# Kernel tuning notes

Measured on AMD Instinct MI355X. Metric: run time of the kernel, lower is better.

## Reference

```python
import jax, jax.numpy as jnp
import numpy as np
from jax import lax

EPS = 1e-5
S_CENTROIDS = 2048
K_NEIGH = 32


def _fps(xyz, S):
    """Farthest point sampling. xyz: (B,N,3) -> idx (B,S) int32."""
    B, N, _ = xyz.shape

    def body(carry, _):
        dist, farthest = carry  # (B,N), (B,)
        centroid = jnp.take_along_axis(xyz, farthest[:, None, None], axis=1)  # (B,1,3)
        d = jnp.sum((xyz - centroid) ** 2, axis=-1)  # (B,N)
        dist = jnp.minimum(dist, d)
        nxt = jnp.argmax(dist, axis=-1).astype(jnp.int32)
        return (dist, nxt), farthest

    init = (jnp.full((B, N), 1e10, xyz.dtype), jnp.zeros((B,), jnp.int32))
    _, idx = lax.scan(body, init, None, length=S)
    return idx.T  # (B,S)


def _knn(q, p, K):
    """q: (B,S,3) queries, p: (B,N,3) points -> idx (B,S,K) of K nearest."""
    d = (jnp.sum(q * q, -1)[:, :, None] + jnp.sum(p * p, -1)[:, None, :]
         - 2.0 * jnp.einsum('bsd,bnd->bsn', q, p))  # (B,S,N) sq dists
    _, idx = lax.top_k(-d, K)
    return idx


def _mlp_layer(x, w, g, b, m, v):
    # x: (B,S,K,Cin); 1x1 conv == channel matmul, then eval-mode BN, then ReLU
    x = jnp.einsum('bskc,oc->bsko', x, w)
    x = (x - m) * (g * lax.rsqrt(v + EPS)) + b
    return jax.nn.relu(x)


def setup_inputs() -> dict:
    key = jax.random.key(0)
    ks = jax.random.split(key, 8)
    B, N, D = 4, 8192, 64
    inp = {
        'xyz': jax.random.normal(ks[0], (B, N, 3), jnp.float32),
        'points': jax.random.normal(ks[1], (B, D, N), jnp.float32),
        'w0': jax.random.normal(ks[2], (64, 67), jnp.float32) * (1.0 / np.sqrt(67)),
        'g0': jnp.ones((64,), jnp.float32), 'b0': jnp.zeros((64,), jnp.float32),
        'm0': jnp.zeros((64,), jnp.float32), 'v0': jnp.ones((64,), jnp.float32),
        'w1': jax.random.normal(ks[3], (64, 64), jnp.float32) * (1.0 / np.sqrt(64)),
        'g1': jnp.ones((64,), jnp.float32), 'b1': jnp.zeros((64,), jnp.float32),
        'm1': jnp.zeros((64,), jnp.float32), 'v1': jnp.ones((64,), jnp.float32),
        'w2': jax.random.normal(ks[4], (128, 64), jnp.float32) * (1.0 / np.sqrt(64)),
        'g2': jnp.ones((128,), jnp.float32), 'b2': jnp.zeros((128,), jnp.float32),
        'm2': jnp.zeros((128,), jnp.float32), 'v2': jnp.ones((128,), jnp.float32),
    }
    return inp


def reference(xyz, points, w0, g0, b0, m0, v0, w1, g1, b1, m1, v1,
              w2, g2, b2, m2, v2):
    B, N, _ = xyz.shape
    S, K = S_CENTROIDS, K_NEIGH

    # FPS centroids (S < N path of the module)
    fps_idx = _fps(xyz, S)                                        # (B,S)
    new_xyz = jnp.take_along_axis(xyz, fps_idx[..., None], axis=1)  # (B,S,3)

    # KNN grouping
    idx = _knn(new_xyz, xyz, K)                                   # (B,S,K)
    grouped_xyz = jnp.take_along_axis(xyz[:, None], idx[..., None], axis=2)  # (B,S,K,3)
    grouped_xyz = grouped_xyz - new_xyz[:, :, None, :]

    # gather neighbor features: points (B,D,N) -> (B,N,D) -> (B,S,K,D)
    pts = jnp.transpose(points, (0, 2, 1))
    neigh = jnp.take_along_axis(pts[:, None], idx[..., None], axis=2)
    grouped = jnp.concatenate([grouped_xyz, neigh], axis=-1)      # (B,S,K,3+D)

    x = _mlp_layer(grouped, w0, g0, b0, m0, v0)
    x = _mlp_layer(x, w1, g1, b1, m1, v1)
    x = _mlp_layer(x, w2, g2, b2, m2, v2)                         # (B,S,K,128)

    new_points = jnp.transpose(jnp.max(x, axis=2), (0, 2, 1))     # (B,128,S)
    return new_xyz, new_points
```

## Files before the change

### kernel.cpp

```cpp
#include <hip/hip_runtime.h>
#include <cfloat>
#include <climits>

#define NPTS   8192
#define SCENT  2048
#define KNEIGH 32
#define BATCH  4
#define DFEAT  64
#define FPS_T  512
#define NV     8
#define NW     8
#define CAP    64
#define NCONS  252
#define CPB    63

typedef float v2f __attribute__((ext_vector_type(2)));

#define DPPTOP2(um, us, ctrl, rmask)                                                  \
    { unsigned _tm = (unsigned)__builtin_amdgcn_update_dpp(0, (int)(um), (ctrl),      \
                                                           (rmask), 0xf, false);     \
      unsigned _ts = (unsigned)__builtin_amdgcn_update_dpp(0, (int)(us), (ctrl),      \
                                                           (rmask), 0xf, false);     \
      unsigned _lo = ((um) < _tm) ? (um) : _tm;                                       \
      (us) = ((us) > _ts) ? (us) : _ts;                                               \
      (us) = ((us) > _lo) ? (us) : _lo;                                               \
      (um) = ((um) > _tm) ? (um) : _tm; }

#define FLUSH_PUB(Eidx, VX, VY, VZ, HASPREV, PX, PY, PZ)                              \
    if (((Eidx) & 63) == 63) {                                                        \
        const int base0 = (Eidx) - 63;                                                \
        if (t < 64 * 3) {                                                             \
            const int ci = base0 + t / 3;                                             \
            const int cc = t - (t / 3) * 3;                                           \
            float v;                                                                  \
            if (ci == (Eidx))                                                         \
                v = (cc == 0) ? (VX) : ((cc == 1) ? (VY) : (VZ));                     \
            else if ((HASPREV) && ci == (Eidx) - 1)                                   \
                v = (cc == 0) ? (PX) : ((cc == 1) ? (PY) : (PZ));                     \
            else                                                                      \
                v = (cc == 0) ? S.hx[ci] : ((cc == 1) ? S.hy[ci] : S.hz[ci]);         \
            __hip_atomic_store(&new_xyz[((size_t)b * SCENT + base0) * 3 + t], v,      \
                               __ATOMIC_RELAXED, __HIP_MEMORY_SCOPE_AGENT);           \
        }                                                                             \
        __syncthreads();                 \
        if (t == 0)                                                                   \
            __hip_atomic_store(&progress[b], (Eidx) + 1,                              \
                               __ATOMIC_RELEASE, __HIP_MEMORY_SCOPE_AGENT);           \
    }

struct FpsSh {
    float sx[NPTS], sy[NPTS], sz[NPTS];
    float hx[SCENT], hy[SCENT], hz[SCENT];
    alignas(16) unsigned slotQ[2][NW][4];
    int scand[CAP];
    int scnt;
    alignas(8) double sdd[2][NW];
    double sfv[NW];
    int sfo[NW];
};
struct ConsSh {
    float  spx[2048], spy[2048], spz[2048];
    double sp2[2048];
    float  tile[32 * 33];
    float  regA[64 * 68];
    float  regB[64 * 64];
    float  regC[128 * 64];
    float  prm[512];
};
union ShU { FpsSh f; ConsSh c; };

__global__ __launch_bounds__(FPS_T, 1) void fused_kernel(
        const float* __restrict__ xyz, float* __restrict__ new_xyz,
        const float* __restrict__ pts, float* __restrict__ ptsT,
        int* __restrict__ progress, int* __restrict__ tcount,
        float* __restrict__ out_points,
        const float* __restrict__ w0, const float* __restrict__ g0,
        const float* __restrict__ b0, const float* __restrict__ m0,
        const float* __restrict__ v0, const float* __restrict__ w1,
        const float* __restrict__ g1, const float* __restrict__ b1,
        const float* __restrict__ m1, const float* __restrict__ v1,
        const float* __restrict__ w2, const float* __restrict__ g2,
        const float* __restrict__ b2, const float* __restrict__ m2,
        const float* __restrict__ v2) {
    __shared__ ShU sh;
    const int t = threadIdx.x;
    const int lane = t & 63, w = t >> 6;

    if (blockIdx.x < BATCH) {
        FpsSh& S = sh.f;
        const int b = blockIdx.x;
        const float* X = xyz + (size_t)b * NPTS * 3;

        for (int p = t; p < NPTS; p += FPS_T) {
            S.sx[p] = X[3 * p + 0]; S.sy[p] = X[3 * p + 1]; S.sz[p] = X[3 * p + 2];
        }

        v2f px2[NV], py2[NV], pz2[NV], dist2[NV];
#pragma unroll
        for (int j = 0; j < NV; ++j) {
            int pA = t + FPS_T * j, pB = t + FPS_T * (j + NV);
            px2[j] = (v2f){X[3 * pA + 0], X[3 * pB + 0]};
            py2[j] = (v2f){X[3 * pA + 1], X[3 * pB + 1]};
            pz2[j] = (v2f){X[3 * pA + 2], X[3 * pB + 2]};
            dist2[j] = (v2f){1e10f, 1e10f};
        }
        float c0x = X[0], c0y = X[1], c0z = X[2];
        float c1x = 0.f, c1y = 0.f, c1z = 0.f;
        int dual = 0, buf = 0;
        int E = 1;
        if (t == 0) { S.hx[0] = c0x; S.hy[0] = c0y; S.hz[0] = c0z; }
        __syncthreads();

#pragma unroll 1
        while (true) {
            float m2s = -1.f, s2s = -1.f;
            {
                const v2f cxx = {c0x, c0x}, cyy = {c0y, c0y}, czz = {c0z, c0z};
                if (dual) {
                    const v2f exx = {c1x, c1x}, eyy = {c1y, c1y}, ezz = {c1z, c1z};
#pragma unroll
                    for (int j = 0; j < NV; ++j) {
                        v2f dx = px2[j] - cxx, dy = py2[j] - cyy, dz = pz2[j] - czz;
                        v2f d0 = __builtin_elementwise_fma(dx, dx,
                                 __builtin_elementwise_fma(dy, dy, dz * dz));
                        v2f ex = px2[j] - exx, ey = py2[j] - eyy, ez = pz2[j] - ezz;
                        v2f d1 = __builtin_elementwise_fma(ex, ex,
                                 __builtin_elementwise_fma(ey, ey, ez * ez));
                        v2f d  = __builtin_elementwise_min(d0, d1);
                        v2f nd = __builtin_elementwise_min(dist2[j], d);
                        dist2[j] = nd;
                        float hi = fmaxf(nd.x, nd.y), lo = fminf(nd.x, nd.y);
                        s2s = fmaxf(fmaxf(s2s, lo), fminf(m2s, hi));
                        m2s = fmaxf(m2s, hi);
                    }
                } else {
#pragma unroll
                    for (int j = 0; j < NV; ++j) {
                        v2f dx = px2[j] - cxx, dy = py2[j] - cyy, dz = pz2[j] - czz;
                        v2f d  = __builtin_elementwise_fma(dx, dx,
                                 __builtin_elementwise_fma(dy, dy, dz * dz));
                        v2f nd = __builtin_elementwise_min(dist2[j], d);
                        dist2[j] = nd;
                        float hi = fmaxf(nd.x, nd.y), lo = fminf(nd.x, nd.y);
                        s2s = fmaxf(fmaxf(s2s, lo), fminf(m2s, hi));
                        m2s = fmaxf(m2s, hi);
                    }
                }
            }
            const float m = m2s, sec = s2s;

            int mi = 0;
#pragma unroll
            for (int j = 0; j < NV; ++j) {
                mi = (dist2[j].x == m) ? (t + FPS_T * j)        : mi;
                mi = (dist2[j].y == m) ? (t + FPS_T * (j + NV)) : mi;
            }

            const unsigned myU = __float_as_uint(m);
            unsigned um = myU, us = __float_as_uint(sec);
            DPPTOP2(um, us, 0x111, 0xf);
            DPPTOP2(um, us, 0x112, 0xf);
            DPPTOP2(um, us, 0x114, 0xf);
            DPPTOP2(um, us, 0x118, 0xf);
            DPPTOP2(um, us, 0x142, 0xa);
            DPPTOP2(um, us, 0x143, 0xc);
            const unsigned wu  = (unsigned)__builtin_amdgcn_readlane((int)um, 63);
            const unsigned wsu = (unsigned)__builtin_amdgcn_readlane((int)us, 63);

            unsigned long long wb = __ballot(myU == wu);
            const int wl   = __ffsll(wb) - 1;
            const int widx = __builtin_amdgcn_readlane(mi, wl);
            const float thwf = __fmul_rn(__uint_as_float(wu), 0.999998f);
            const unsigned tw = (__uint_as_float(wsu) >= thwf) ? 1u : 0u;
            if (lane == 0) {
                *(uint4*)&S.slotQ[buf][w][0] =
                    make_uint4(wu, (unsigned)widx | (tw << 14), wsu, 0u);
            }
            __syncthreads();

            unsigned mv[NW], mt4[NW], sv2[NW];
            {
                const uint4* qp = (const uint4*)&S.slotQ[buf][0][0];
                uint4 u0 = qp[0], u1 = qp[1], u2 = qp[2], u3 = qp[3];
                uint4 u4 = qp[4], u5 = qp[5], u6 = qp[6], u7 = qp[7];
                mv[0]=u0.x; mt4[0]=u0.y; sv2[0]=u0.z;
                mv[1]=u1.x; mt4[1]=u1.y; sv2[1]=u1.z;
                mv[2]=u2.x; mt4[2]=u2.y; sv2[2]=u2.z;
                mv[3]=u3.x; mt4[3]=u3.y; sv2[3]=u3.z;
                mv[4]=u4.x; mt4[4]=u4.y; sv2[4]=u4.z;
                mv[5]=u5.x; mt4[5]=u5.y; sv2[5]=u5.z;
                mv[6]=u6.x; mt4[6]=u6.y; sv2[6]=u6.z;
                mv[7]=u7.x; mt4[7]=u7.y; sv2[7]=u7.z;
            }
            unsigned gu = mv[0];
#pragma unroll
            for (int k = 1; k < NW; ++k) gu = (mv[k] > gu) ? mv[k] : gu;
            const float gvf  = __uint_as_float(gu);
            const float gthf = __fmul_rn(gvf, 0.999998f);
            const unsigned ugth = __float_as_uint(gthf);
            int nw = 0; unsigned meta = 0; int kw = 0;
#pragma unroll
            for (int k = NW - 1; k >= 0; --k) {
                nw  += (mv[k] >= ugth) ? 1 : 0;
                meta = (mv[k] == gu) ? mt4[k] : meta;
                kw   = (mv[k] == gu) ? k : kw;
            }
            const int wtie = (meta >> 14) & 1;
            int i1 = (int)(meta & 0x3fffu);
            const int fb = (nw >= 2) || wtie;

            if (fb) {
                if (t == 0) S.scnt = 0;
                __syncthreads();
#pragma unroll
                for (int j = 0; j < NV; ++j) {
                    if (dist2[j].x >= gthf) {
                        int slot = atomicAdd(&S.scnt, 1);
                        if (slot < CAP) S.scand[slot] = t + FPS_T * j;
                    }
                    if (dist2[j].y >= gthf) {
                        int slot = atomicAdd(&S.scnt, 1);
                        if (slot < CAP) S.scand[slot] = t + FPS_T * (j + NV);
                    }
                }
                __syncthreads();
                const int mm = S.scnt;
                if (mm <= CAP) {
                    double bd = -1.0; int bi = INT_MAX;
#pragma unroll 1
                    for (int k = 0; k < mm; ++k) {
                        const int pos = S.scand[k];
                        const double pxd = (double)S.sx[pos], pyd = (double)S.sy[pos],
                                     pzd = (double)S.sz[pos];
                        double dd = 1e10;
                        for (int i = t; i < E; i += FPS_T) {
                            double ddx = __dsub_rn(pxd, (double)S.hx[i]);
                            double ddy = __dsub_rn(pyd, (double)S.hy[i]);
                            double ddz = __dsub_rn(pzd, (double)S.hz[i]);
                            double d = __dadd_rn(__dadd_rn(__dmul_rn(ddx, ddx), __dmul_rn(ddy, ddy)),
                                                 __dmul_rn(ddz, ddz));
                            dd = fmin(dd, d);
                        }
#pragma unroll
                        for (int off = 32; off >= 1; off >>= 1)
                            dd = fmin(dd, __shfl_down(dd, off));
                        if (lane == 0) S.sdd[k & 1][w] = dd;
                        __syncthreads();
                        double ddm = S.sdd[k & 1][0];
#pragma unroll
                        for (int w2i = 1; w2i < NW; ++w2i) ddm = fmin(ddm, S.sdd[k & 1][w2i]);
                        if (ddm > bd || (ddm == bd && pos < bi)) { bd = ddm; bi = pos; }
                    }
                    i1 = bi;
                } else {
                    double bv = -1.0; int bi = INT_MAX;
#pragma unroll 1
                    for (int j = 0; j < 2 * NV; ++j) {
                        const int jj = j & (NV - 1);
                        const bool hiHalf = j >= NV;
                        const double pxd = (double)(hiHalf ? px2[jj].y : px2[jj].x);
                        const double pyd = (double)(hiHalf ? py2[jj].y : py2[jj].x);
                        const double pzd = (double)(hiHalf ? pz2[jj].y : pz2[jj].x);
                        double dd = 1e10;
                        for (int i = 0; i < E; ++i) {
                            double ddx = __dsub_rn(pxd, (double)S.hx[i]);
                            double ddy = __dsub_rn(pyd, (double)S.hy[i]);
                            double ddz = __dsub_rn(pzd, (double)S.hz[i]);
                            double d = __dadd_rn(__dadd_rn(__dmul_rn(ddx, ddx), __dmul_rn(ddy, ddy)),
                                                 __dmul_rn(ddz, ddz));
                            dd = fmin(dd, d);
                        }
                        int pidx = t + FPS_T * j;
                        if (dd > bv || (dd == bv && pidx < bi)) { bv = dd; bi = pidx; }
                    }
#pragma unroll
                    for (int off = 32; off >= 1; off >>= 1) {
                        double ov = __shfl_down(bv, off);
                        int    oi = __shfl_down(bi, off);
                        if (ov > bv || (ov == bv && oi < bi)) { bv = ov; bi = oi; }
                    }
                    if (lane == 0) { S.sfv[w] = bv; S.sfo[w] = bi; }
                    __syncthreads();
                    bv = S.sfv[0]; bi = S.sfo[0];
#pragma unroll
                    for (int w2i = 1; w2i < NW; ++w2i) {
                        double ov = S.sfv[w2i]; int oi = S.sfo[w2i];
                        if (ov > bv || (ov == bv && oi < bi)) { bv = ov; bi = oi; }
                    }
                    i1 = bi;
                }
                __syncthreads();
            }

            const float e0x = S.sx[i1], e0y = S.sy[i1], e0z = S.sz[i1];
            if (t == 0) { S.hx[E] = e0x; S.hy[E] = e0y; S.hz[E] = e0z; }
            FLUSH_PUB(E, e0x, e0y, e0z, 0, 0.f, 0.f, 0.f);
            c0x = e0x; c0y = e0y; c0z = e0z;

            int peeled = 0;
            float e1x = 0.f, e1y = 0.f, e1z = 0.f;
            if (!fb && (E + 1) < SCENT) {
                unsigned arr[NW];
#pragma unroll
                for (int k = 0; k < NW; ++k) arr[k] = (k == kw) ? sv2[k] : mv[k];
                unsigned v2u = arr[0];
#pragma unroll
                for (int k = 1; k < NW; ++k) v2u = (arr[k] > v2u) ? arr[k] : v2u;
                int k2 = 0; unsigned meta2 = 0;
#pragma unroll
                for (int k = NW - 1; k >= 0; --k) {
                    meta2 = (arr[k] == v2u) ? mt4[k] : meta2;
                    k2    = (arr[k] == v2u) ? k : k2;
                }
                unsigned v3u = 0;
#pragma unroll
                for (int k = 0; k < NW; ++k) {
                    const unsigned cnd = (k == kw || k == k2) ? sv2[k] : mv[k];
                    v3u = (cnd > v3u) ? cnd : v3u;
                }
                const float v2vf = __uint_as_float(v2u);
                const float v3vf = __uint_as_float(v3u);
                const int i2 = (int)(meta2 & 0x3fffu);
                e1x = S.sx[i2]; e1y = S.sy[i2]; e1z = S.sz[i2];
                const float ddx = e1x - e0x, ddy = e1y - e0y, ddz = e1z - e0z;
                const float dq = fmaf(ddx, ddx, fmaf(ddy, ddy, ddz * ddz));
                const float wnew = fminf(v2vf, dq);
                peeled = ((k2 != kw) &&
                          (wnew > __fmul_rn(v3vf, 1.000004f))) ? 1 : 0;
            }
            if (peeled) {
                const int e1i = E + 1;
                if (t == 0) { S.hx[e1i] = e1x; S.hy[e1i] = e1y; S.hz[e1i] = e1z; }
                FLUSH_PUB(e1i, e1x, e1y, e1z, 1, e0x, e0y, e0z);
                c1x = e1x; c1y = e1y; c1z = e1z;
                dual = 1;
                E = e1i + 1;
            } else {
                dual = 0;
                E = E + 1;
            }
            if (E >= SCENT) break;
            buf ^= 1;
        }
    } else {
        ConsSh& K = sh.c;
        const int local = blockIdx.x - BATCH;
        const int batch = local / CPB;
        const int cl    = local % CPB;
        const int tx = t & 31, ty = t >> 5;

        for (int tid2 = local; tid2 < 2048; tid2 += NCONS) {
            const int bt = tid2 >> 9, rest = tid2 & 511;
            const int d0 = (rest >> 8) * 32, n0 = (rest & 255) * 32;
            __syncthreads();
#pragma unroll
            for (int i = 0; i < 2; ++i)
                K.tile[(ty + 16 * i) * 33 + tx] =
                    pts[(size_t)bt * DFEAT * NPTS + (size_t)(d0 + ty + 16 * i) * NPTS + n0 + tx];
            __syncthreads();
#pragma unroll
            for (int i = 0; i < 2; ++i)
                ptsT[(size_t)bt * NPTS * DFEAT + (size_t)(n0 + ty + 16 * i) * DFEAT + d0 + tx] =
                    K.tile[tx * 33 + ty + 16 * i];
        }
        if (t == 0) {
            __threadfence();
            atomicAdd(tcount, 1);
        }

        for (int idx = t; idx < 64 * 68; idx += FPS_T) {
            int o = idx / 68, i = idx - o * 68;
            float v;
            if (i < 64)      v = w0[o * 67 + 3 + i];
            else if (i < 67) v = w0[o * 67 + (i - 64)];
            else             v = 0.0f;
            K.regA[idx] = v;
        }
        for (int idx = t; idx < 64 * 64; idx += FPS_T)  K.regB[idx] = w1[idx];
        for (int idx = t; idx < 128 * 64; idx += FPS_T) K.regC[idx] = w2[idx];
        if (t < 64) {
            float a0v = g0[t] / sqrtf(v0[t] + 1e-5f);
            K.prm[t]       = a0v;
            K.prm[64 + t]  = b0[t] - m0[t] * a0v;
            float a1v = g1[t] / sqrtf(v1[t] + 1e-5f);
            K.prm[128 + t] = a1v;
            K.prm[192 + t] = b1[t] - m1[t] * a1v;
        } else if (t < 192) {
            int o = t - 64;
            float a2v = g2[o] / sqrtf(v2[o] + 1e-5f);
            K.prm[256 + o] = a2v;
            K.prm[384 + o] = b2[o] - m2[o] * a2v;
        }

        const float* Xb = xyz + (size_t)batch * NPTS * 3;
#pragma unroll 1
        for (int r = 0; ; ++r) {
            const int sBase = r * (CPB * NW) + cl * NW;
            if (sBase >= SCENT) break;
            const int sMax = min(sBase + NW - 1, SCENT - 1);
            if (t == 0) {
                while (__hip_atomic_load(&progress[batch], __ATOMIC_ACQUIRE,
                                         __HIP_MEMORY_SCOPE_AGENT) < sMax + 1)
                    __builtin_amdgcn_s_sleep(8);
                if (r == 0) {
                    while (__hip_atomic_load(tcount, __ATOMIC_ACQUIRE,
                                             __HIP_MEMORY_SCOPE_AGENT) < NCONS)
                        __builtin_amdgcn_s_sleep(8);
                }
            }
            __syncthreads();

            const int sQ = min(sBase + w, SCENT - 1);
            const float* q = new_xyz + ((size_t)batch * SCENT + sQ) * 3;
            const float qfx = q[0], qfy = q[1], qfz = q[2];
            const double qx = (double)qfx, qy = (double)qfy, qz = (double)qfz;
            const double q2 = __dadd_rn(__dadd_rn(__dmul_rn(qx, qx), __dmul_rn(qy, qy)),
                                        __dmul_rn(qz, qz));

            double ld   = DBL_MAX;
            int    li   = 0x7fffffff;
            double taud = DBL_MAX;
            int    taui = 0x7fffffff;

#pragma unroll 1
            for (int c = 0; c < 4; ++c) {
                __syncthreads();
#pragma unroll
                for (int r2 = 0; r2 < 4; ++r2) {
                    int pl = r2 * 512 + t;
                    int p  = c * 2048 + pl;
                    float x = Xb[3 * p + 0], y = Xb[3 * p + 1], z = Xb[3 * p + 2];
                    K.spx[pl] = x; K.spy[pl] = y; K.spz[pl] = z;
                    double dx = (double)x, dy = (double)y, dz = (double)z;
                    K.sp2[pl] = __dadd_rn(__dadd_rn(__dmul_rn(dx, dx), __dmul_rn(dy, dy)),
                                          __dmul_rn(dz, dz));
                }
                __syncthreads();
#pragma unroll 1
                for (int i = 0; i < 32; ++i) {
                    const int pl   = i * 64 + lane;
                    const int pidx = c * 2048 + pl;
                    double px = (double)K.spx[pl], py = (double)K.spy[pl],
                           pz = (double)K.spz[pl];
                    double qp = __dadd_rn(__dadd_rn(__dmul_rn(qx, px), __dmul_rn(qy, py)),
                                          __dmul_rn(qz, pz));
                    double d  = __dsub_rn(__dadd_rn(q2, K.sp2[pl]), __dmul_rn(2.0, qp));
                    bool cand = (d < taud) || (d == taud && pidx < taui);
                    unsigned long long mmask = __ballot(cand);
                    while (mmask) {
                        int sl = __ffsll((unsigned long long)mmask) - 1;
                        mmask &= mmask - 1;
                        double dv = __shfl(d, sl);
                        int    iv = __shfl(pidx, sl);
                        if (dv < taud || (dv == taud && iv < taui)) {
                            bool gt = (lane < 32) && (ld > dv || (ld == dv && li > iv));
                            unsigned long long gm = __ballot(gt);
                            double ud = __shfl_up(ld, 1);
                            int    ui = __shfl_up(li, 1);
                            if (gt) { ld = ud; li = ui; }
                            bool first = gt && ((lane == 0) || !((gm >> (lane - 1)) & 1ull));
                            if (first) { ld = dv; li = iv; }
                            taud = __shfl(ld, 31);
                            taui = __shfl(li, 31);
                        }
                    }
                }
            }

            if (sBase + w < SCENT && lane < 32) {
                const int nidx = li;
                const float* P3 = Xb + (size_t)nidx * 3;
                const float dx = P3[0] - qfx, dy = P3[1] - qfy, dz = P3[2] - qfz;

                const float4* F = (const float4*)(ptsT + ((size_t)batch * NPTS + nidx) * 64);
                float4 xv[17];
#pragma unroll
                for (int i = 0; i < 16; ++i) xv[i] = F[i];
                xv[16] = make_float4(dx, dy, dz, 0.0f);

                float h0[64];
                const float4* W0 = (const float4*)K.regA;
#pragma unroll
                for (int o = 0; o < 64; ++o) {
                    float acc = 0.f;
#pragma unroll
                    for (int i = 0; i < 17; ++i) {
                        float4 ww = W0[o * 17 + i];
                        acc = fmaf(xv[i].x, ww.x, acc);
                        acc = fmaf(xv[i].y, ww.y, acc);
                        acc = fmaf(xv[i].z, ww.z, acc);
                        acc = fmaf(xv[i].w, ww.w, acc);
                    }
                    h0[o] = fmaxf(fmaf(acc, K.prm[o], K.prm[64 + o]), 0.f);
                }
                float h1[64];
                const float4* W1 = (const float4*)K.regB;
#pragma unroll
                for (int o = 0; o < 64; ++o) {
                    float acc = 0.f;
#pragma unroll
                    for (int i = 0; i < 16; ++i) {
                        float4 ww = W1[o * 16 + i];
                        acc = fmaf(h0[4 * i + 0], ww.x, acc);
                        acc = fmaf(h0[4 * i + 1], ww.y, acc);
                        acc = fmaf(h0[4 * i + 2], ww.z, acc);
                        acc = fmaf(h0[4 * i + 3], ww.w, acc);
                    }
                    h1[o] = fmaxf(fmaf(acc, K.prm[128 + o], K.prm[192 + o]), 0.f);
                }
                const float4* W2 = (const float4*)K.regC;
                float* outp = out_points + (size_t)batch * 128 * SCENT + sQ;
#pragma unroll 1
                for (int o = 0; o < 128; ++o) {
                    float acc = 0.f;
#pragma unroll
                    for (int i = 0; i < 16; ++i) {
                        float4 ww = W2[o * 16 + i];
                        acc = fmaf(h1[4 * i + 0], ww.x, acc);
                        acc = fmaf(h1[4 * i + 1], ww.y, acc);
                        acc = fmaf(h1[4 * i + 2], ww.z, acc);
                        acc = fmaf(h1[4 * i + 3], ww.w, acc);
                    }
                    float y = fmaxf(fmaf(acc, K.prm[256 + o], K.prm[384 + o]), 0.f);
#pragma unroll
                    for (int off = 16; off >= 1; off >>= 1)
                        y = fmaxf(y, __shfl_xor(y, off));
                    if (lane == 0) outp[(size_t)o * SCENT] = y;
                }
            }
        }
    }
}

extern "C" void kernel_launch(void* const* d_in, const int* in_sizes, int n_in,
                              void* d_out, int out_size, void* d_ws, size_t ws_size,
                              hipStream_t stream) {
    const float* xyz    = (const float*)d_in[0];
    const float* points = (const float*)d_in[1];
    const float* w0 = (const float*)d_in[2];
    const float* g0 = (const float*)d_in[3];
    const float* b0 = (const float*)d_in[4];
    const float* m0 = (const float*)d_in[5];
    const float* v0 = (const float*)d_in[6];
    const float* w1 = (const float*)d_in[7];
    const float* g1 = (const float*)d_in[8];
    const float* b1 = (const float*)d_in[9];
    const float* m1 = (const float*)d_in[10];
    const float* v1 = (const float*)d_in[11];
    const float* w2 = (const float*)d_in[12];
    const float* g2 = (const float*)d_in[13];
    const float* b2 = (const float*)d_in[14];
    const float* m2 = (const float*)d_in[15];
    const float* v2 = (const float*)d_in[16];

    float* out_xyz    = (float*)d_out;
    float* out_points = (float*)d_out + (size_t)BATCH * SCENT * 3;

    char* ws = (char*)d_ws;
    int*   progress = (int*)ws;
    int*   tcount   = (int*)(ws + 64);
    float* ptsT     = (float*)(ws + 32768);

    hipMemsetAsync(ws, 0, 128, stream);

    void* kargs[] = { (void*)&xyz, (void*)&out_xyz, (void*)&points, (void*)&ptsT,
                      (void*)&progress, (void*)&tcount, (void*)&out_points,
                      (void*)&w0, (void*)&g0, (void*)&b0, (void*)&m0, (void*)&v0,
                      (void*)&w1, (void*)&g1, (void*)&b1, (void*)&m1, (void*)&v1,
                      (void*)&w2, (void*)&g2, (void*)&b2, (void*)&m2, (void*)&v2 };
    hipLaunchCooperativeKernel((const void*)fused_kernel,
                               dim3(BATCH + NCONS), dim3(FPS_T), kargs, 0, stream);
}
```

Measured before the change: 2.252 ms.

## Extend speculative FPS peeling to commit up to three centroids per iteration

Extends the farthest-point-sampling loop so that, after accepting a second speculative centroid, it also tries a third. The candidate comes from another wave's maximum and is accepted when its updated distance provably beats every remaining wave's second-best value. When that holds, the next distance-update pass folds in three centroids in one sweep, which removes another full block-wide argmax reduction and its barriers from the serial chain. The cost is extra scalar checks, more live registers, and a third distance variant in the unrolled loop, which may raise register pressure.

```diff
diff --git a/kernel.cpp b/kernel.cpp
--- a/kernel.cpp
+++ b/kernel.cpp
@@ -26,7 +26,7 @@
       (us) = ((us) > _lo) ? (us) : _lo;                                               \
       (um) = ((um) > _tm) ? (um) : _tm; }
 
-#define FLUSH_PUB(Eidx, VX, VY, VZ, HASPREV, PX, PY, PZ)                              \
+#define FLUSH_PUBN(Eidx, VX, VY, VZ, NPREV, P1X, P1Y, P1Z, P2X, P2Y, P2Z)             \
     if (((Eidx) & 63) == 63) {                                                        \
         const int base0 = (Eidx) - 63;                                                \
         if (t < 64 * 3) {                                                             \
@@ -35,8 +35,10 @@
             float v;                                                                  \
             if (ci == (Eidx))                                                         \
                 v = (cc == 0) ? (VX) : ((cc == 1) ? (VY) : (VZ));                     \
-            else if ((HASPREV) && ci == (Eidx) - 1)                                   \
-                v = (cc == 0) ? (PX) : ((cc == 1) ? (PY) : (PZ));                     \
+            else if ((NPREV) >= 1 && ci == (Eidx) - 1)                                \
+                v = (cc == 0) ? (P1X) : ((cc == 1) ? (P1Y) : (P1Z));                  \
+            else if ((NPREV) >= 2 && ci == (Eidx) - 2)                                \
+                v = (cc == 0) ? (P2X) : ((cc == 1) ? (P2Y) : (P2Z));                  \
             else                                                                      \
                 v = (cc == 0) ? S.hx[ci] : ((cc == 1) ? S.hy[ci] : S.hz[ci]);         \
             __hip_atomic_store(&new_xyz[((size_t)b * SCENT + base0) * 3 + t], v,      \
@@ -106,7 +108,8 @@
         }
         float c0x = X[0], c0y = X[1], c0z = X[2];
         float c1x = 0.f, c1y = 0.f, c1z = 0.f;
-        int dual = 0, buf = 0;
+        float c2x = 0.f, c2y = 0.f, c2z = 0.f;
+        int pend = 0, buf = 0;
         int E = 1;
         if (t == 0) { S.hx[0] = c0x; S.hy[0] = c0y; S.hz[0] = c0z; }
         __syncthreads();
@@ -116,7 +119,19 @@
             float m2s = -1.f, s2s = -1.f;
             {
                 const v2f cxx = {c0x, c0x}, cyy = {c0y, c0y}, czz = {c0z, c0z};
-                if (dual) {
+                if (pend == 0) {
+#pragma unroll
+                    for (int j = 0; j < NV; ++j) {
+                        v2f dx = px2[j] - cxx, dy = py2[j] - cyy, dz = pz2[j] - czz;
+                        v2f d  = __builtin_elementwise_fma(dx, dx,
+                                 __builtin_elementwise_fma(dy, dy, dz * dz));
+                        v2f nd = __builtin_elementwise_min(dist2[j], d);
+                        dist2[j] = nd;
+                        float hi = fmaxf(nd.x, nd.y), lo = fminf(nd.x, nd.y);
+                        s2s = fmaxf(fmaxf(s2s, lo), fminf(m2s, hi));
+                        m2s = fmaxf(m2s, hi);
+                    }
+                } else if (pend == 1) {
                     const v2f exx = {c1x, c1x}, eyy = {c1y, c1y}, ezz = {c1z, c1z};
 #pragma unroll
                     for (int j = 0; j < NV; ++j) {
@@ -134,11 +149,21 @@
                         m2s = fmaxf(m2s, hi);
                     }
                 } else {
+                    const v2f exx = {c1x, c1x}, eyy = {c1y, c1y}, ezz = {c1z, c1z};
+                    const v2f fxx = {c2x, c2x}, fyy = {c2y, c2y}, fzz = {c2z, c2z};
 #pragma unroll
                     for (int j = 0; j < NV; ++j) {
                         v2f dx = px2[j] - cxx, dy = py2[j] - cyy, dz = pz2[j] - czz;
-                        v2f d  = __builtin_elementwise_fma(dx, dx,
+                        v2f d0 = __builtin_elementwise_fma(dx, dx,
                                  __builtin_elementwise_fma(dy, dy, dz * dz));
+                        v2f ex = px2[j] - exx, ey = py2[j] - eyy, ez = pz2[j] - ezz;
+                        v2f d1 = __builtin_elementwise_fma(ex, ex,
+                                 __builtin_elementwise_fma(ey, ey, ez * ez));
+                        v2f fx = px2[j] - fxx, fy = py2[j] - fyy, fz = pz2[j] - fzz;
+                        v2f d2 = __builtin_elementwise_fma(fx, fx,
+                                 __builtin_elementwise_fma(fy, fy, fz * fz));
+                        v2f d  = __builtin_elementwise_min(
+                                     __builtin_elementwise_min(d0, d1), d2);
                         v2f nd = __builtin_elementwise_min(dist2[j], d);
                         dist2[j] = nd;
                         float hi = fmaxf(nd.x, nd.y), lo = fminf(nd.x, nd.y);
@@ -294,11 +319,13 @@
 
             const float e0x = S.sx[i1], e0y = S.sy[i1], e0z = S.sz[i1];
             if (t == 0) { S.hx[E] = e0x; S.hy[E] = e0y; S.hz[E] = e0z; }
-            FLUSH_PUB(E, e0x, e0y, e0z, 0, 0.f, 0.f, 0.f);
+            FLUSH_PUBN(E, e0x, e0y, e0z, 0, 0.f, 0.f, 0.f, 0.f, 0.f, 0.f);
             c0x = e0x; c0y = e0y; c0z = e0z;
 
             int peeled = 0;
             float e1x = 0.f, e1y = 0.f, e1z = 0.f;
+            int kw_s = kw, k2_s = 0;
+            unsigned v3u = 0;
             if (!fb && (E + 1) < SCENT) {
                 unsigned arr[NW];
 #pragma unroll
@@ -312,7 +339,6 @@
                     meta2 = (arr[k] == v2u) ? mt4[k] : meta2;
                     k2    = (arr[k] == v2u) ? k : k2;
                 }
-                unsigned v3u = 0;
 #pragma unroll
                 for (int k = 0; k < NW; ++k) {
                     const unsigned cnd = (k == kw || k == k2) ? sv2[k] : mv[k];
@@ -327,16 +353,55 @@
                 const float wnew = fminf(v2vf, dq);
                 peeled = ((k2 != kw) &&
                           (wnew > __fmul_rn(v3vf, 1.000004f))) ? 1 : 0;
+                k2_s = k2;
             }
             if (peeled) {
                 const int e1i = E + 1;
                 if (t == 0) { S.hx[e1i] = e1x; S.hy[e1i] = e1y; S.hz[e1i] = e1z; }
-                FLUSH_PUB(e1i, e1x, e1y, e1z, 1, e0x, e0y, e0z);
+                FLUSH_PUBN(e1i, e1x, e1y, e1z, 1, e0x, e0y, e0z, 0.f, 0.f, 0.f);
                 c1x = e1x; c1y = e1y; c1z = e1z;
-                dual = 1;
-                E = e1i + 1;
+
+                int peel3 = 0;
+                float e2xx = 0.f, e2yy = 0.f, e2zz = 0.f;
+                if ((E + 2) < SCENT) {
+                    int k3 = -1;
+#pragma unroll
+                    for (int k = NW - 1; k >= 0; --k)
+                        if (k != kw_s && k != k2_s && mv[k] == v3u) k3 = k;
+                    if (k3 >= 0) {
+                        unsigned v4u = 0;
+#pragma unroll
+                        for (int k = 0; k < NW; ++k) {
+                            const unsigned cnd =
+                                (k == kw_s || k == k2_s || k == k3) ? sv2[k] : mv[k];
+                            v4u = (cnd > v4u) ? cnd : v4u;
+                        }
+                        const int i3 = (int)(mt4[k3] & 0x3fffu);
+                        e2xx = S.sx[i3]; e2yy = S.sy[i3]; e2zz = S.sz[i3];
+                        const float ax = e2xx - e0x, ay = e2yy - e0y, az = e2zz - e0z;
+                        const float dq03 = fmaf(ax, ax, fmaf(ay, ay, az * az));
+                        const float bx = e2xx - e1x, by = e2yy - e1y, bz = e2zz - e1z;
+                        const float dq13 = fmaf(bx, bx, fmaf(by, by, bz * bz));
+                        const float wnew3 =
+                            fminf(fminf(__uint_as_float(v3u), dq03), dq13);
+                        peel3 = (wnew3 >
+                                 __fmul_rn(__uint_as_float(v4u), 1.000004f)) ? 1 : 0;
+                    }
+                }
+                if (peel3) {
+                    const int e2i = E + 2;
+                    if (t == 0) { S.hx[e2i] = e2xx; S.hy[e2i] = e2yy; S.hz[e2i] = e2zz; }
+                    FLUSH_PUBN(e2i, e2xx, e2yy, e2zz, 2,
+                               e1x, e1y, e1z, e0x, e0y, e0z);
+                    c2x = e2xx; c2y = e2yy; c2z = e2zz;
+                    pend = 2;
+                    E = e2i + 1;
+                } else {
+                    pend = 1;
+                    E = e1i + 1;
+                }
             } else {
-                dual = 0;
+                pend = 0;
                 E = E + 1;
             }
             if (E >= SCENT) break;
```

New measurement: 2.295 ms. About the same (+1.9%).
